# Optimization experiments

Hardware: AMD Instinct MI355X
Metric: run time of the kernel (lower is better)

The kernel has to match this reference:

```python
import jax, jax.numpy as jnp
import numpy as np

IMAGE_SIZE = 256
PSIZE = 8
STRIDE = 4
WINDOW = IMAGE_SIZE + 1 - PSIZE  # 249


def _build_indices():
    # replicate image2patch.__init__ mask construction
    cur = np.arange(0, WINDOW, STRIDE)
    if cur[-1] != WINDOW - 1:
        cur = np.append(cur, WINDOW - 1)
    grid = np.arange(WINDOW * WINDOW).reshape(WINDOW, WINDOW)
    mask = grid[np.ix_(cur, cur)].reshape(-1)  # [M] window-origin flat indices
    rows = mask // WINDOW  # [M] patch top-left row
    cols = mask % WINDOW   # [M] patch top-left col
    k = np.arange(PSIZE * PSIZE)
    di, dj = k // PSIZE, k % PSIZE  # offsets within patch; flat index k = i*PSIZE + j
    r_full = rows[:, None] + di[None, :]  # [M, PSIZE^2]
    c_full = cols[:, None] + dj[None, :]  # [M, PSIZE^2]
    return jnp.asarray(r_full, dtype=jnp.int32), jnp.asarray(c_full, dtype=jnp.int32)

R_IDX, C_IDX = _build_indices()


def setup_inputs() -> dict:
    key = jax.random.key(0)
    x = jax.random.normal(key, (32, 8, IMAGE_SIZE, IMAGE_SIZE), dtype=jnp.float32)
    return {"input_data": x}


def reference(input_data):
    # output[b*c, m, i*PSIZE+j] = input_data[b, c, rows[m]+i, cols[m]+j]
    B, C, H, W = input_data.shape
    x = input_data.reshape(B * C, H, W)
    out = x[:, R_IDX, C_IDX]  # [B*C, M, PSIZE^2] vectorized sliding-window gather
    return out
```

## Files before the change

### kernel.cpp

```cpp
#include <hip/hip_runtime.h>


constexpr unsigned NPDIM   = 63;
constexpr unsigned PATCHES = NPDIM * NPDIM;
constexpr unsigned CHUNKS  = 16;
constexpr unsigned ROWPAD  = 65;

using fv4 = __attribute__((ext_vector_type(4))) float;

__global__ __launch_bounds__(256) void image2patch_kernel(
    const fv4* __restrict__ in4, fv4* __restrict__ out4) {
    __shared__ fv4 lds4[8 * ROWPAD];

    unsigned bid = blockIdx.x;
    unsigned n   = bid / NPDIM;
    unsigned pr  = bid - n * NPDIM;

    unsigned inbase4 = n * 16384u + pr * 256u;
    unsigned t = threadIdx.x;
    {
        unsigned r0 = t >> 6, c0 = t & 63u;
        lds4[r0 * ROWPAD + c0] = in4[inbase4 + t];
        unsigned i1 = t + 256u;
        unsigned r1 = i1 >> 6, c1 = i1 & 63u;
        lds4[r1 * ROWPAD + c1] = in4[inbase4 + i1];
    }
    __syncthreads();

    unsigned outbase4 = (n * PATCHES + pr * NPDIM) * CHUNKS;
    #pragma unroll
    for (unsigned it = 0; it < 4; ++it) {
        unsigned i = it * 256u + t;
        if (i < NPDIM * CHUNKS) {
            unsigned pc  = i >> 4;
            unsigned k4  = i & 15u;
            unsigned di  = k4 >> 1;
            unsigned dj4 = k4 & 1u;
            fv4 v = lds4[di * ROWPAD + pc + dj4];
            __builtin_nontemporal_store(v, &out4[outbase4 + i]);
        }
    }
}

extern "C" void kernel_launch(void* const* d_in, const int* in_sizes, int n_in,
                              void* d_out, int out_size, void* d_ws, size_t ws_size,
                              hipStream_t stream) {
    const fv4* in4 = (const fv4*)d_in[0];
    fv4* out4 = (fv4*)d_out;
    unsigned blocks = 256u * NPDIM;
    image2patch_kernel<<<blocks, 256, 0, stream>>>(in4, out4);
}
```

Baseline: 295.2 us.

## Process bands of three patch rows per block with XCD-aware block swizzle

Each block now loads a 16-row input band into LDS and emits three patch rows, so overlapping input rows between adjacent patch rows are read once instead of twice. This cuts redundant global reads and reduces the block count threefold. A block-index swizzle groups consecutive bands onto the same XCD to improve L2 locality. The cost is a larger LDS footprint and more work per block, with fewer blocks available to hide latency.

New measurement: 301.8 us. 1.02x slower.

```diff
diff --git a/kernel.cpp b/kernel.cpp
--- a/kernel.cpp
+++ b/kernel.cpp
@@ -4,40 +4,48 @@
 constexpr unsigned NPDIM   = 63;
 constexpr unsigned PATCHES = NPDIM * NPDIM;
 constexpr unsigned CHUNKS  = 16;
+constexpr unsigned PB      = 3;
+constexpr unsigned BANDS   = NPDIM / PB;
+constexpr unsigned SROWS   = 4 * PB + 4;
 constexpr unsigned ROWPAD  = 65;
 
 using fv4 = __attribute__((ext_vector_type(4))) float;
 
 __global__ __launch_bounds__(256) void image2patch_kernel(
     const fv4* __restrict__ in4, fv4* __restrict__ out4) {
-    __shared__ fv4 lds4[8 * ROWPAD];
+    __shared__ fv4 lds4[SROWS * ROWPAD];
 
+    unsigned cpx = gridDim.x >> 3;
     unsigned bid = blockIdx.x;
-    unsigned n   = bid / NPDIM;
-    unsigned pr  = bid - n * NPDIM;
+    unsigned swz = (bid & 7u) * cpx + (bid >> 3);
 
-    unsigned inbase4 = n * 16384u + pr * 256u;
+    unsigned n  = swz / BANDS;
+    unsigned pb = swz - n * BANDS;
+
     unsigned t = threadIdx.x;
-    {
-        unsigned r0 = t >> 6, c0 = t & 63u;
-        lds4[r0 * ROWPAD + c0] = in4[inbase4 + t];
-        unsigned i1 = t + 256u;
-        unsigned r1 = i1 >> 6, c1 = i1 & 63u;
-        lds4[r1 * ROWPAD + c1] = in4[inbase4 + i1];
+
+    unsigned inbase4 = n * 16384u + pb * (12u * 64u);
+    #pragma unroll
+    for (unsigned k = 0; k < 4; ++k) {
+        unsigned idx = k * 256u + t;
+        lds4[(idx >> 6) * ROWPAD + (idx & 63u)] = in4[inbase4 + idx];
     }
     __syncthreads();
 
-    unsigned outbase4 = (n * PATCHES + pr * NPDIM) * CHUNKS;
     #pragma unroll
-    for (unsigned it = 0; it < 4; ++it) {
-        unsigned i = it * 256u + t;
-        if (i < NPDIM * CHUNKS) {
-            unsigned pc  = i >> 4;
-            unsigned k4  = i & 15u;
-            unsigned di  = k4 >> 1;
-            unsigned dj4 = k4 & 1u;
-            fv4 v = lds4[di * ROWPAD + pc + dj4];
-            __builtin_nontemporal_store(v, &out4[outbase4 + i]);
+    for (unsigned prl = 0; prl < PB; ++prl) {
+        unsigned outbase4 = (n * PATCHES + (pb * PB + prl) * NPDIM) * CHUNKS;
+        #pragma unroll
+        for (unsigned it = 0; it < 4; ++it) {
+            unsigned i = it * 256u + t;
+            if (i < NPDIM * CHUNKS) {
+                unsigned pc  = i >> 4;
+                unsigned k4  = i & 15u;
+                unsigned di  = k4 >> 1;
+                unsigned dj4 = k4 & 1u;
+                fv4 v = lds4[(4u * prl + di) * ROWPAD + pc + dj4];
+                __builtin_nontemporal_store(v, &out4[outbase4 + i]);
+            }
         }
     }
 }
@@ -47,6 +55,6 @@
                               hipStream_t stream) {
     const fv4* in4 = (const fv4*)d_in[0];
     fv4* out4 = (fv4*)d_out;
-    unsigned blocks = 256u * NPDIM;
+    unsigned blocks = 256u * BANDS;
     image2patch_kernel<<<blocks, 256, 0, stream>>>(in4, out4);
 }
```
